# Kernel tuning notes

Measured on AMD Instinct MI355X. Metric: run time of the kernel, lower is better.

The kernel has to match this reference:

```python
import jax, jax.numpy as jnp
import numpy as np

MIN_EXPERT_CAPACITY = 4
EPS = 1e-9
CAPACITY_FACTOR = 2.0  # eval capacity factor


def cumsum_exclusive(t, axis):
    return jnp.cumsum(t, axis=axis) - t


def safe_one_hot(idx, depth):
    # one_hot with an extra slot so idx == depth maps to nothing, then slice
    return jax.nn.one_hot(idx, depth + 1)[..., :depth]


def setup_inputs() -> dict:
    key = jax.random.key(0)
    k_x, k_g, k_w1, k_w2 = jax.random.split(key, 4)
    b, n, d, e, h = 2, 4096, 512, 16, 2048
    x = jax.random.normal(k_x, (b, n, d), dtype=jnp.float32)
    w_gating = jax.random.normal(k_g, (d, e), dtype=jnp.float32) / np.sqrt(d)
    w1 = jax.random.normal(k_w1, (e, d, h), dtype=jnp.float32) / np.sqrt(d)
    w2 = jax.random.normal(k_w2, (e, h, d), dtype=jnp.float32) / np.sqrt(h)
    return {"x": x, "w_gating": w_gating, "w1": w1, "w2": w2}


def top2_gating(x, w_gating):
    b, n, d = x.shape
    e = w_gating.shape[-1]
    raw_gates = jax.nn.softmax(jnp.einsum('bnd,de->bne', x, w_gating), axis=-1)

    gate_1 = jnp.max(raw_gates, axis=-1)
    index_1 = jnp.argmax(raw_gates, axis=-1)
    mask_1 = jax.nn.one_hot(index_1, e, dtype=raw_gates.dtype)

    gates_without_top1 = raw_gates * (1.0 - mask_1)
    gate_2 = jnp.max(gates_without_top1, axis=-1)
    index_2 = jnp.argmax(gates_without_top1, axis=-1)
    mask_2 = jax.nn.one_hot(index_2, e, dtype=raw_gates.dtype)

    denom = gate_1 + gate_2 + EPS
    gate_1 = gate_1 / denom
    gate_2 = gate_2 / denom

    # load-balancing loss
    density_1 = jnp.mean(mask_1, axis=-2)
    density_1_proxy = jnp.mean(raw_gates, axis=-2)
    loss = jnp.mean(density_1_proxy * density_1) * float(e * e)

    # second policy == 'all' -> keep mask_2 as-is

    capacity = max(min(n, int((n * 2) * CAPACITY_FACTOR / e)), MIN_EXPERT_CAPACITY)
    cap_f = float(capacity)

    pos1 = cumsum_exclusive(mask_1, axis=-2) * mask_1  # [b,n,e]
    mask_1 = mask_1 * (pos1 < cap_f).astype(mask_1.dtype)
    mask_1_count = jnp.sum(mask_1, axis=-2, keepdims=True)
    mask_1_flat = jnp.sum(mask_1, axis=-1)  # [b,n]
    pos1 = jnp.sum(pos1, axis=-1)
    gate_1 = gate_1 * mask_1_flat

    pos2 = (cumsum_exclusive(mask_2, axis=-2) + mask_1_count) * mask_2
    mask_2 = mask_2 * (pos2 < cap_f).astype(mask_2.dtype)
    mask_2_flat = jnp.sum(mask_2, axis=-1)
    pos2 = jnp.sum(pos2, axis=-1)
    gate_2 = gate_2 * mask_2_flat

    # combine tensor: [b, n, e, c]
    combine = (gate_1[..., None, None] * mask_1_flat[..., None, None]
               * jax.nn.one_hot(index_1, e, dtype=x.dtype)[..., None]
               * safe_one_hot(pos1.astype(jnp.int32), capacity)[..., None, :]
               + gate_2[..., None, None] * mask_2_flat[..., None, None]
               * jax.nn.one_hot(index_2, e, dtype=x.dtype)[..., None]
               * safe_one_hot(pos2.astype(jnp.int32), capacity)[..., None, :])
    dispatch = (combine > 0).astype(combine.dtype)
    return dispatch, combine, loss


def reference(x, w_gating, w1, w2):
    dispatch, combine, loss = top2_gating(x, w_gating)
    # dispatch: gather tokens into expert buckets [e, b, c, d]
    expert_inputs = jnp.einsum('bnd,bnec->ebcd', x, dispatch)
    # expert FFN (eval mode: dropout is identity)
    hidden = jax.nn.relu(jnp.einsum('ebcd,edh->ebch', expert_inputs, w1))
    expert_outputs = jnp.einsum('ebch,ehd->ebcd', hidden, w2)
    # combine back to token order, weighted by gate values
    output = jnp.einsum('ebcd,bnec->bnd', expert_outputs, combine)
    return output
```

## Files before the change

### kernel.cpp

```cpp
#include <hip/hip_runtime.h>

#define BB 2
#define NN 4096
#define DD 512
#define EE 16
#define HH 2048
#define CAP 1024
#define NTOK (BB*NN)
#define MM (BB*CAP)
#define MAXSTRIP 160

typedef unsigned short ushort_t;
typedef __attribute__((ext_vector_type(8))) short bf16x8;
typedef __attribute__((ext_vector_type(4))) float floatx4;

__device__ __forceinline__ ushort_t f2bf(float f) {
    union { float f; unsigned u; } v; v.f = f;
    unsigned r = v.u + 0x7fffu + ((v.u >> 16) & 1u);
    return (ushort_t)(r >> 16);
}

__device__ __forceinline__ void cp16(const void* g, void* l) {
    __builtin_amdgcn_global_load_lds(
        (const __attribute__((address_space(1))) void*)g,
        (__attribute__((address_space(3))) void*)l, 16, 0, 0);
}

__launch_bounds__(256)
__global__ void gating_kernel(const float* __restrict__ x,
                              const float* __restrict__ wg,
                              int* __restrict__ e1, int* __restrict__ e2,
                              float* __restrict__ g1, float* __restrict__ g2,
                              ushort_t* __restrict__ xbf) {
    int wave = threadIdx.x >> 6;
    int lane = threadIdx.x & 63;
    int t = blockIdx.x * 4 + wave;
    const float* xp = x + (size_t)t * DD;

    float4 xa = ((const float4*)xp)[lane * 2];
    float4 xb = ((const float4*)xp)[lane * 2 + 1];
    float xs[8] = {xa.x, xa.y, xa.z, xa.w, xb.x, xb.y, xb.z, xb.w};

    ushort4 h0, h1;
    h0.x = f2bf(xs[0]); h0.y = f2bf(xs[1]); h0.z = f2bf(xs[2]); h0.w = f2bf(xs[3]);
    h1.x = f2bf(xs[4]); h1.y = f2bf(xs[5]); h1.z = f2bf(xs[6]); h1.w = f2bf(xs[7]);
    ushort4* xo = (ushort4*)(xbf + (size_t)t * DD);
    xo[lane * 2] = h0; xo[lane * 2 + 1] = h1;

    float acc[EE];
#pragma unroll
    for (int e = 0; e < EE; e++) acc[e] = 0.f;
    int d0 = lane * 8;
#pragma unroll
    for (int j = 0; j < 8; j++) {
        const float* wrow = wg + (d0 + j) * EE;
#pragma unroll
        for (int e = 0; e < EE; e++) acc[e] = fmaf(xs[j], wrow[e], acc[e]);
    }
#pragma unroll
    for (int off = 32; off > 0; off >>= 1) {
#pragma unroll
        for (int e = 0; e < EE; e++) acc[e] += __shfl_xor(acc[e], off, 64);
    }
    if (lane == 0) {
        float m = acc[0];
#pragma unroll
        for (int e = 1; e < EE; e++) m = fmaxf(m, acc[e]);
        float p[EE]; float s = 0.f;
#pragma unroll
        for (int e = 0; e < EE; e++) { p[e] = __expf(acc[e] - m); s += p[e]; }
        float inv = 1.f / s;
#pragma unroll
        for (int e = 0; e < EE; e++) p[e] *= inv;
        int i1 = 0; float v1 = p[0];
#pragma unroll
        for (int e = 1; e < EE; e++) if (p[e] > v1) { v1 = p[e]; i1 = e; }
        int i2 = (i1 == 0) ? 1 : 0; float v2 = p[i2];
#pragma unroll
        for (int e = 0; e < EE; e++)
            if (e != i1 && p[e] > v2) { v2 = p[e]; i2 = e; }
        float denom = v1 + v2 + 1e-9f;
        e1[t] = i1; e2[t] = i2;
        g1[t] = v1 / denom; g2[t] = v2 / denom;
    }
}

__launch_bounds__(256)
__global__ void scan_kernel(const int* __restrict__ e1, const int* __restrict__ e2,
                            const float* __restrict__ g1, const float* __restrict__ g2,
                            int* __restrict__ s2t, float* __restrict__ s2g,
                            int* __restrict__ used) {
    int b = blockIdx.x / EE;
    int e = blockIdx.x % EE;
    int tid = threadIdx.x;
    const int base = b * NN;
    int n0 = tid * 16;

    unsigned m1 = 0, m2 = 0;
    int c1 = 0, c2 = 0;
#pragma unroll
    for (int j = 0; j < 16; j++) {
        int n = n0 + j;
        if (e1[base + n] == e) { m1 |= 1u << j; c1++; }
        if (e2[base + n] == e) { m2 |= 1u << j; c2++; }
    }
    __shared__ int s1[256], s2[256];
    __shared__ int s_used;
    s1[tid] = c1; s2[tid] = c2;
    __syncthreads();
    for (int off = 1; off < 256; off <<= 1) {
        int a1 = (tid >= off) ? s1[tid - off] : 0;
        int a2 = (tid >= off) ? s2[tid - off] : 0;
        __syncthreads();
        s1[tid] += a1; s2[tid] += a2;
        __syncthreads();
    }
    int total1 = s1[255];
    int total2 = s2[255];
    int kept1 = min(total1, CAP);
    int ex1 = s1[tid] - c1;
    int ex2 = s2[tid] - c2 + kept1;
    const int sbase = (e * BB + b) * CAP;
#pragma unroll
    for (int j = 0; j < 16; j++) {
        int n = n0 + j;
        if (m1 & (1u << j)) {
            if (ex1 < CAP) { s2t[sbase + ex1] = base + n; s2g[sbase + ex1] = g1[base + n]; }
            ex1++;
        }
        if (m2 & (1u << j)) {
            if (ex2 < CAP) { s2t[sbase + ex2] = base + n; s2g[sbase + ex2] = g2[base + n]; }
            ex2++;
        }
    }
    if (tid == 255) {
        int kept2 = min(total2, max(0, CAP - kept1));
        int u = kept1 + kept2;
        used[e * BB + b] = u;
        s_used = u;
    }
    __syncthreads();
    for (int i = s_used + tid; i < CAP; i += 256) s2t[sbase + i] = -1;
}

__global__ void schedule_kernel(const int* __restrict__ used, int* __restrict__ meta) {
    __shared__ int ns[32], pre[32];
    int i = threadIdx.x;
    if (i < 32) {
        int e = i >> 1, b = i & 1;
        ns[i] = (used[e * BB + b] + 127) >> 7;
    }
    __syncthreads();
    if (i == 0) {
        int acc = 0;
        for (int j = 0; j < 32; j++) { pre[j] = acc; acc += ns[j]; }
    }
    __syncthreads();
    if (i < 16) {
        int e = i;
        int xcd = e & 7;
        int mine  = ns[2 * e] + ns[2 * e + 1];
        int po    = (e < 8) ? (e + 8) : (e - 8);
        int other = ns[2 * po] + ns[2 * po + 1];
        if (e < 8) {
            meta[xcd]     = (mine + other) * 16;
            meta[8 + xcd] = (mine + other) * 4;
        }
        int off = (e < 8) ? 0 : other;
        int* sc1 = meta + 16 + xcd * 512 + off * 16;
        int j = 0;
        for (int col = 0; col < 16; col++)
            for (int bb = 0; bb < 2; bb++)
                for (int s = 0; s < ns[2 * e + bb]; s++) {
                    int wi = pre[2 * e + bb] + s;
                    sc1[j++] = (e << 17) | (wi << 9) | ((bb * 8 + s) << 5) | col;
                }
        int* sc2 = meta + 16 + 4096 + xcd * 128 + off * 4;
        j = 0;
        for (int col = 0; col < 4; col++)
            for (int bb = 0; bb < 2; bb++)
                for (int s = 0; s < ns[2 * e + bb]; s++) {
                    int wi = pre[2 * e + bb] + s;
                    sc2[j++] = (e << 17) | (wi << 9) | ((bb * 8 + s) << 5) | col;
                }
    }
}

__global__ void transpose_bf16(const float* __restrict__ in,
                               ushort_t* __restrict__ outp, int R, int C) {
    __shared__ float tile[32][33];
    const float* slab = in + (size_t)blockIdx.z * R * C;
    ushort_t* oslab = outp + (size_t)blockIdx.z * R * C;
    int c0 = blockIdx.x * 32, r0 = blockIdx.y * 32;
    int tx = threadIdx.x, ty = threadIdx.y;
#pragma unroll
    for (int j = 0; j < 4; j++)
        tile[ty + j * 8][tx] = slab[(size_t)(r0 + ty + j * 8) * C + c0 + tx];
    __syncthreads();
#pragma unroll
    for (int j = 0; j < 4; j++)
        oslab[(size_t)(c0 + ty + j * 8) * R + r0 + tx] = f2bf(tile[tx][ty + j * 8]);
}

template <int MODE>
__launch_bounds__(256)
__global__ void gemm_mfma(const ushort_t* __restrict__ Abase,
                          const ushort_t* __restrict__ Bt,
                          void* __restrict__ Cout,
                          const int* __restrict__ meta,
                          const int* __restrict__ s2t,
                          const float* __restrict__ s2g) {
    constexpr int K = (MODE == 0) ? DD : HH;
    constexpr int KITERS = K / 32;

    int xcd = blockIdx.x;
    if ((int)blockIdx.y >= meta[(MODE == 0 ? 0 : 8) + xcd]) return;
    int job = meta[16 + (MODE == 0 ? 0 : 4096) + xcd * (MODE == 0 ? 512 : 128) + blockIdx.y];
    int col0  = (job & 31) * 128;
    int ytile = (job >> 5) & 15;
    int wi    = (job >> 9) & 255;
    int e     = job >> 17;

    __shared__ ushort_t As[2][128 * 32];
    __shared__ ushort_t Bs[2][128 * 32];

    int tid = threadIdx.x;
    int lane = tid & 63;
    int wid = tid >> 6;
    int wave_m = (wid & 1) << 6;
    int wave_n = (wid >> 1) << 6;
    int lm = lane & 15;
    int quad = lane >> 4;
    int sw = (quad ^ ((lm >> 1) & 3)) * 8;

    const ushort_t* ga[2];
    const ushort_t* gb[2];
#pragma unroll
    for (int it = 0; it < 2; it++) {
        int idx = it * 256 + tid;
        int r = idx >> 2;
        int cg = (idx & 3) ^ ((r >> 1) & 3);
        if (MODE == 0) {
            int tok = s2t[e * MM + ytile * 128 + r];
            if (tok < 0) tok = 0;
            ga[it] = Abase + (size_t)tok * DD + cg * 8;
        } else {
            ga[it] = Abase + (size_t)(wi * 128 + r) * HH + cg * 8;
        }
        gb[it] = Bt + (size_t)e * HH * DD + (size_t)(col0 + r) * K + cg * 8;
    }

    auto stage = [&](int buf, int ki) {
#pragma unroll
        for (int it = 0; it < 2; it++)
            cp16(ga[it] + ki * 32, &As[buf][(it * 256 + tid) * 8]);
#pragma unroll
        for (int it = 0; it < 2; it++)
            cp16(gb[it] + ki * 32, &Bs[buf][(it * 256 + tid) * 8]);
    };

    floatx4 acc[4][4];
#pragma unroll
    for (int i = 0; i < 4; i++)
#pragma unroll
        for (int j = 0; j < 4; j++)
            acc[i][j] = (floatx4)(0.f);

    stage(0, 0);
#pragma unroll 2
    for (int ki = 0; ki < KITERS; ki++) {
        int cur = ki & 1;
        if (ki + 1 < KITERS) {
            stage(cur ^ 1, ki + 1);
            asm volatile("s_waitcnt vmcnt(4)\ns_barrier" ::: "memory");
        } else {
            asm volatile("s_waitcnt vmcnt(0)\ns_barrier" ::: "memory");
        }
        bf16x8 af[4], bfr[4];
#pragma unroll
        for (int mt = 0; mt < 4; mt++)
            af[mt] = *(const bf16x8*)&As[cur][(wave_m + mt * 16 + lm) * 32 + sw];
#pragma unroll
        for (int nt = 0; nt < 4; nt++)
            bfr[nt] = *(const bf16x8*)&Bs[cur][(wave_n + nt * 16 + lm) * 32 + sw];
#pragma unroll
        for (int mt = 0; mt < 4; mt++)
#pragma unroll
            for (int nt = 0; nt < 4; nt++)
                acc[mt][nt] = __builtin_amdgcn_mfma_f32_16x16x32_bf16(
                    af[mt], bfr[nt], acc[mt][nt], 0, 0, 0);
        asm volatile("s_waitcnt lgkmcnt(0)\ns_barrier" ::: "memory");
    }

    if (MODE == 0) {
        ushort_t* hp = (ushort_t*)Cout + (size_t)wi * 128 * HH;
#pragma unroll
        for (int mt = 0; mt < 4; mt++) {
#pragma unroll
            for (int r = 0; r < 4; r++) {
                int row = wave_m + mt * 16 + quad * 4 + r;
#pragma unroll
                for (int nt = 0; nt < 4; nt++) {
                    int col = col0 + wave_n + nt * 16 + lm;
                    hp[(size_t)row * HH + col] = f2bf(fmaxf(acc[mt][nt][r], 0.f));
                }
            }
        }
    } else {
        float* outp = (float*)Cout;
#pragma unroll
        for (int mt = 0; mt < 4; mt++) {
#pragma unroll
            for (int r = 0; r < 4; r++) {
                int row = wave_m + mt * 16 + quad * 4 + r;
                int slot = e * MM + ytile * 128 + row;
                int tok = s2t[slot];
                if (tok < 0) continue;
                float g = s2g[slot];
#pragma unroll
                for (int nt = 0; nt < 4; nt++) {
                    int col = col0 + wave_n + nt * 16 + lm;
                    atomicAdd(outp + (size_t)tok * DD + col, g * acc[mt][nt][r]);
                }
            }
        }
    }
}

extern "C" void kernel_launch(void* const* d_in, const int* in_sizes, int n_in,
                              void* d_out, int out_size, void* d_ws, size_t ws_size,
                              hipStream_t stream) {
    const float* x  = (const float*)d_in[0];
    const float* wg = (const float*)d_in[1];
    const float* w1 = (const float*)d_in[2];
    const float* w2 = (const float*)d_in[3];
    float* out = (float*)d_out;

    char* ws = (char*)d_ws;
    int*      e1   = (int*)(ws);
    int*      e2   = (int*)(ws + 32768);
    float*    g1   = (float*)(ws + 65536);
    float*    g2   = (float*)(ws + 98304);
    int*      used = (int*)(ws + 131072);
    int*      meta = (int*)(ws + 132096);
    int*      s2t  = (int*)(ws + 152704);
    float*    s2g  = (float*)(ws + 283776);
    ushort_t* xbf  = (ushort_t*)(ws + 414848);
    ushort_t* wt   = (ushort_t*)(ws + 8803456);
    ushort_t* hid  = (ushort_t*)(ws + 42357888);

    hipMemsetAsync(out, 0, (size_t)NTOK * DD * sizeof(float), stream);

    gating_kernel<<<NTOK / 4, 256, 0, stream>>>(x, wg, e1, e2, g1, g2, xbf);
    scan_kernel<<<BB * EE, 256, 0, stream>>>(e1, e2, g1, g2, s2t, s2g, used);
    schedule_kernel<<<1, 64, 0, stream>>>(used, meta);

    transpose_bf16<<<dim3(HH / 32, DD / 32, EE), dim3(32, 8), 0, stream>>>(w1, wt, DD, HH);
    gemm_mfma<0><<<dim3(8, 512), 256, 0, stream>>>(xbf, wt, hid, meta, s2t, s2g);

    transpose_bf16<<<dim3(DD / 32, HH / 32, EE), dim3(32, 8), 0, stream>>>(w2, wt, HH, DD);
    gemm_mfma<1><<<dim3(8, 128), 256, 0, stream>>>(hid, wt, out, meta, s2t, s2g);
}
```

Before: 366.6 us.

## Fuse expert FFN GEMMs into one kernel keeping hidden chunks in LDS

Replaces the two separate expert GEMM launches, and the bf16 hidden tensor round trip through global memory, with one fused kernel. Each 512-thread block owns a 128-row token tile of one expert, computes 256-wide hidden chunks into swizzled LDS, and accumulates the second GEMM in registers. The schedule becomes one job per token tile, and the weight transpose uses 64x64 tiles with float2 loads. In exchange, the grid is far smaller (at most a few dozen active blocks), LDS use is large and the accumulators take many registers, so the GPU may be underused.

```diff
diff --git a/kernel.cpp b/kernel.cpp
--- a/kernel.cpp
+++ b/kernel.cpp
@@ -8,7 +8,6 @@
 #define CAP 1024
 #define NTOK (BB*NN)
 #define MM (BB*CAP)
-#define MAXSTRIP 160
 
 typedef unsigned short ushort_t;
 typedef __attribute__((ext_vector_type(8))) short bf16x8;
@@ -144,187 +143,203 @@
 }
 
 __global__ void schedule_kernel(const int* __restrict__ used, int* __restrict__ meta) {
-    __shared__ int ns[32], pre[32];
-    int i = threadIdx.x;
-    if (i < 32) {
-        int e = i >> 1, b = i & 1;
-        ns[i] = (used[e * BB + b] + 127) >> 7;
-    }
-    __syncthreads();
-    if (i == 0) {
-        int acc = 0;
-        for (int j = 0; j < 32; j++) { pre[j] = acc; acc += ns[j]; }
-    }
-    __syncthreads();
-    if (i < 16) {
-        int e = i;
-        int xcd = e & 7;
-        int mine  = ns[2 * e] + ns[2 * e + 1];
-        int po    = (e < 8) ? (e + 8) : (e - 8);
-        int other = ns[2 * po] + ns[2 * po + 1];
-        if (e < 8) {
-            meta[xcd]     = (mine + other) * 16;
-            meta[8 + xcd] = (mine + other) * 4;
-        }
-        int off = (e < 8) ? 0 : other;
-        int* sc1 = meta + 16 + xcd * 512 + off * 16;
-        int j = 0;
-        for (int col = 0; col < 16; col++)
-            for (int bb = 0; bb < 2; bb++)
-                for (int s = 0; s < ns[2 * e + bb]; s++) {
-                    int wi = pre[2 * e + bb] + s;
-                    sc1[j++] = (e << 17) | (wi << 9) | ((bb * 8 + s) << 5) | col;
-                }
-        int* sc2 = meta + 16 + 4096 + xcd * 128 + off * 4;
-        j = 0;
-        for (int col = 0; col < 4; col++)
-            for (int bb = 0; bb < 2; bb++)
-                for (int s = 0; s < ns[2 * e + bb]; s++) {
-                    int wi = pre[2 * e + bb] + s;
-                    sc2[j++] = (e << 17) | (wi << 9) | ((bb * 8 + s) << 5) | col;
-                }
-    }
+    int x = threadIdx.x;
+    if (x >= 8) return;
+    int cnt = 0;
+#pragma unroll
+    for (int ei = 0; ei < 2; ei++) {
+        int e = x + ei * 8;
+        for (int b = 0; b < 2; b++) {
+            int ns = (used[e * BB + b] + 127) >> 7;
+            for (int s = 0; s < ns; s++)
+                meta[8 + x * 32 + cnt++] = (e << 8) | ((e * BB + b) * 8 + s);
+        }
+    }
+    meta[x] = cnt;
 }
 
 __global__ void transpose_bf16(const float* __restrict__ in,
                                ushort_t* __restrict__ outp, int R, int C) {
-    __shared__ float tile[32][33];
+    __shared__ float tile[64][65];
     const float* slab = in + (size_t)blockIdx.z * R * C;
     ushort_t* oslab = outp + (size_t)blockIdx.z * R * C;
-    int c0 = blockIdx.x * 32, r0 = blockIdx.y * 32;
+    int c0 = blockIdx.x * 64, r0 = blockIdx.y * 64;
     int tx = threadIdx.x, ty = threadIdx.y;
 #pragma unroll
-    for (int j = 0; j < 4; j++)
-        tile[ty + j * 8][tx] = slab[(size_t)(r0 + ty + j * 8) * C + c0 + tx];
+    for (int j = 0; j < 8; j++) {
+        int r = ty + j * 8;
+        float2 v = *(const float2*)&slab[(size_t)(r0 + r) * C + c0 + tx * 2];
+        tile[r][tx * 2] = v.x; tile[r][tx * 2 + 1] = v.y;
+    }
     __syncthreads();
 #pragma unroll
-    for (int j = 0; j < 4; j++)
-        oslab[(size_t)(c0 + ty + j * 8) * R + r0 + tx] = f2bf(tile[tx][ty + j * 8]);
-}
-
-template <int MODE>
-__launch_bounds__(256)
-__global__ void gemm_mfma(const ushort_t* __restrict__ Abase,
-                          const ushort_t* __restrict__ Bt,
-                          void* __restrict__ Cout,
+    for (int j = 0; j < 8; j++) {
+        int c = ty + j * 8;
+        ushort2 h;
+        h.x = f2bf(tile[tx * 2][c]);
+        h.y = f2bf(tile[tx * 2 + 1][c]);
+        *(ushort2*)&oslab[(size_t)(c0 + c) * R + r0 + tx * 2] = h;
+    }
+}
+
+__launch_bounds__(512)
+__global__ void fused_ffn(const ushort_t* __restrict__ xbf,
+                          const ushort_t* __restrict__ w1t,
+                          const ushort_t* __restrict__ w2t,
+                          float* __restrict__ outp,
                           const int* __restrict__ meta,
                           const int* __restrict__ s2t,
                           const float* __restrict__ s2g) {
-    constexpr int K = (MODE == 0) ? DD : HH;
-    constexpr int KITERS = K / 32;
-
     int xcd = blockIdx.x;
-    if ((int)blockIdx.y >= meta[(MODE == 0 ? 0 : 8) + xcd]) return;
-    int job = meta[16 + (MODE == 0 ? 0 : 4096) + xcd * (MODE == 0 ? 512 : 128) + blockIdx.y];
-    int col0  = (job & 31) * 128;
-    int ytile = (job >> 5) & 15;
-    int wi    = (job >> 9) & 255;
-    int e     = job >> 17;
-
-    __shared__ ushort_t As[2][128 * 32];
-    __shared__ ushort_t Bs[2][128 * 32];
-
-    int tid = threadIdx.x;
-    int lane = tid & 63;
-    int wid = tid >> 6;
-    int wave_m = (wid & 1) << 6;
-    int wave_n = (wid >> 1) << 6;
-    int lm = lane & 15;
-    int quad = lane >> 4;
-    int sw = (quad ^ ((lm >> 1) & 3)) * 8;
-
-    const ushort_t* ga[2];
-    const ushort_t* gb[2];
-#pragma unroll
-    for (int it = 0; it < 2; it++) {
-        int idx = it * 256 + tid;
-        int r = idx >> 2;
-        int cg = (idx & 3) ^ ((r >> 1) & 3);
-        if (MODE == 0) {
-            int tok = s2t[e * MM + ytile * 128 + r];
-            if (tok < 0) tok = 0;
-            ga[it] = Abase + (size_t)tok * DD + cg * 8;
-        } else {
-            ga[it] = Abase + (size_t)(wi * 128 + r) * HH + cg * 8;
-        }
-        gb[it] = Bt + (size_t)e * HH * DD + (size_t)(col0 + r) * K + cg * 8;
-    }
-
-    auto stage = [&](int buf, int ki) {
-#pragma unroll
-        for (int it = 0; it < 2; it++)
-            cp16(ga[it] + ki * 32, &As[buf][(it * 256 + tid) * 8]);
-#pragma unroll
-        for (int it = 0; it < 2; it++)
-            cp16(gb[it] + ki * 32, &Bs[buf][(it * 256 + tid) * 8]);
-    };
-
-    floatx4 acc[4][4];
+    if ((int)blockIdx.y >= meta[xcd]) return;
+    int job = meta[8 + xcd * 32 + blockIdx.y];
+    int e = job >> 8;
+    int slot0 = (job & 255) << 7;
+
+    __shared__ ushort_t Ats[2][128 * 32];
+    __shared__ ushort_t Wts[2][512 * 32];
+    __shared__ ushort_t Hs[128 * 256];
+
+    const int tid = threadIdx.x;
+    const int lane = tid & 63;
+    const int wid = tid >> 6;
+    const int lm = lane & 15;
+    const int quad = lane >> 4;
+    const int swz = (quad ^ ((lm >> 1) & 3)) * 8;
+
+    const int mh   = (wid & 1) << 6;
+    const int g1_n = (wid >> 1) << 6;
+    const int g2_n = (wid >> 1) << 7;
+
+    int arow = tid >> 2;
+    int tokA = s2t[slot0 + arow];
+    const ushort_t* gA = xbf + (size_t)(tokA < 0 ? 0 : tokA) * DD
+                             + ((tid & 3) ^ ((arow >> 1) & 3)) * 8;
+    const ushort_t* w1b = w1t + ((size_t)e << 20);
+    const ushort_t* w2b = w2t + ((size_t)e << 20);
+    int r0 = tid >> 2, r1 = 128 + (tid >> 2);
+    const ushort_t* gW1a = w1b + (size_t)r0 * DD + ((tid & 3) ^ ((r0 >> 1) & 3)) * 8;
+    const ushort_t* gW1b = w1b + (size_t)r1 * DD + ((tid & 3) ^ ((r1 >> 1) & 3)) * 8;
+    const ushort_t* gW2[4];
+#pragma unroll
+    for (int it = 0; it < 4; it++) {
+        int r = it * 128 + (tid >> 2);
+        gW2[it] = w2b + (size_t)r * HH + ((tid & 3) ^ ((r >> 1) & 3)) * 8;
+    }
+
+    floatx4 acc[4][8];
 #pragma unroll
     for (int i = 0; i < 4; i++)
 #pragma unroll
-        for (int j = 0; j < 4; j++)
+        for (int j = 0; j < 8; j++)
             acc[i][j] = (floatx4)(0.f);
 
-    stage(0, 0);
-#pragma unroll 2
-    for (int ki = 0; ki < KITERS; ki++) {
-        int cur = ki & 1;
-        if (ki + 1 < KITERS) {
-            stage(cur ^ 1, ki + 1);
-            asm volatile("s_waitcnt vmcnt(4)\ns_barrier" ::: "memory");
-        } else {
-            asm volatile("s_waitcnt vmcnt(0)\ns_barrier" ::: "memory");
-        }
-        bf16x8 af[4], bfr[4];
+    for (int chunk = 0; chunk < HH / 256; chunk++) {
+        floatx4 acch[4][4];
+#pragma unroll
+        for (int i = 0; i < 4; i++)
+#pragma unroll
+            for (int j = 0; j < 4; j++)
+                acch[i][j] = (floatx4)(0.f);
+        {
+            const ushort_t* p1 = gW1a + ((size_t)chunk << 17);
+            const ushort_t* p2 = gW1b + ((size_t)chunk << 17);
+            cp16(gA, &Ats[0][tid * 8]);
+            cp16(p1, &Wts[0][tid * 8]);
+            cp16(p2, &Wts[0][(512 + tid) * 8]);
+            for (int kk = 0; kk < 16; kk++) {
+                int cur = kk & 1;
+                if (kk < 15) {
+                    int nx = cur ^ 1, ko = (kk + 1) * 32;
+                    cp16(gA + ko, &Ats[nx][tid * 8]);
+                    cp16(p1 + ko, &Wts[nx][tid * 8]);
+                    cp16(p2 + ko, &Wts[nx][(512 + tid) * 8]);
+                    asm volatile("s_waitcnt vmcnt(3)\ns_barrier" ::: "memory");
+                } else {
+                    asm volatile("s_waitcnt vmcnt(0)\ns_barrier" ::: "memory");
+                }
+                bf16x8 af[4];
+#pragma unroll
+                for (int mt = 0; mt < 4; mt++)
+                    af[mt] = *(const bf16x8*)&Ats[cur][(mh + mt * 16 + lm) * 32 + swz];
+#pragma unroll
+                for (int nt = 0; nt < 4; nt++) {
+                    bf16x8 bf = *(const bf16x8*)&Wts[cur][(g1_n + nt * 16 + lm) * 32 + swz];
+#pragma unroll
+                    for (int mt = 0; mt < 4; mt++)
+                        acch[mt][nt] = __builtin_amdgcn_mfma_f32_16x16x32_bf16(
+                            af[mt], bf, acch[mt][nt], 0, 0, 0);
+                }
+                asm volatile("s_waitcnt lgkmcnt(0)\ns_barrier" ::: "memory");
+            }
+        }
 #pragma unroll
         for (int mt = 0; mt < 4; mt++)
-            af[mt] = *(const bf16x8*)&As[cur][(wave_m + mt * 16 + lm) * 32 + sw];
-#pragma unroll
-        for (int nt = 0; nt < 4; nt++)
-            bfr[nt] = *(const bf16x8*)&Bs[cur][(wave_n + nt * 16 + lm) * 32 + sw];
-#pragma unroll
-        for (int mt = 0; mt < 4; mt++)
 #pragma unroll
             for (int nt = 0; nt < 4; nt++)
-                acc[mt][nt] = __builtin_amdgcn_mfma_f32_16x16x32_bf16(
-                    af[mt], bfr[nt], acc[mt][nt], 0, 0, 0);
+#pragma unroll
+                for (int r = 0; r < 4; r++) {
+                    int row = mh + mt * 16 + quad * 4 + r;
+                    int col = g1_n + nt * 16 + lm;
+                    int ch = (col >> 3) ^ (row & 15);
+                    Hs[row * 256 + ch * 8 + (col & 7)] =
+                        f2bf(fmaxf(acch[mt][nt][r], 0.f));
+                }
         asm volatile("s_waitcnt lgkmcnt(0)\ns_barrier" ::: "memory");
-    }
-
-    if (MODE == 0) {
-        ushort_t* hp = (ushort_t*)Cout + (size_t)wi * 128 * HH;
-#pragma unroll
-        for (int mt = 0; mt < 4; mt++) {
-#pragma unroll
-            for (int r = 0; r < 4; r++) {
-                int row = wave_m + mt * 16 + quad * 4 + r;
-#pragma unroll
-                for (int nt = 0; nt < 4; nt++) {
-                    int col = col0 + wave_n + nt * 16 + lm;
-                    hp[(size_t)row * HH + col] = f2bf(fmaxf(acc[mt][nt][r], 0.f));
-                }
+
+        {
+            size_t co = (size_t)chunk << 8;
+            cp16(gW2[0] + co, &Wts[0][tid * 8]);
+            cp16(gW2[1] + co, &Wts[0][(512 + tid) * 8]);
+            cp16(gW2[2] + co, &Wts[0][(1024 + tid) * 8]);
+            cp16(gW2[3] + co, &Wts[0][(1536 + tid) * 8]);
+            for (int kk = 0; kk < 8; kk++) {
+                int cur = kk & 1;
+                if (kk < 7) {
+                    int nx = cur ^ 1; size_t ko = co + (kk + 1) * 32;
+                    cp16(gW2[0] + ko, &Wts[nx][tid * 8]);
+                    cp16(gW2[1] + ko, &Wts[nx][(512 + tid) * 8]);
+                    cp16(gW2[2] + ko, &Wts[nx][(1024 + tid) * 8]);
+                    cp16(gW2[3] + ko, &Wts[nx][(1536 + tid) * 8]);
+                    asm volatile("s_waitcnt vmcnt(4)\ns_barrier" ::: "memory");
+                } else {
+                    asm volatile("s_waitcnt vmcnt(0)\ns_barrier" ::: "memory");
+                }
+                bf16x8 ah[4];
+#pragma unroll
+                for (int mt = 0; mt < 4; mt++) {
+                    int row = mh + mt * 16 + lm;
+                    int ch = ((kk << 2) + quad) ^ lm;
+                    ah[mt] = *(const bf16x8*)&Hs[row * 256 + ch * 8];
+                }
+#pragma unroll
+                for (int nt = 0; nt < 8; nt++) {
+                    bf16x8 bf = *(const bf16x8*)&Wts[cur][(g2_n + nt * 16 + lm) * 32 + swz];
+#pragma unroll
+                    for (int mt = 0; mt < 4; mt++)
+                        acc[mt][nt] = __builtin_amdgcn_mfma_f32_16x16x32_bf16(
+                            ah[mt], bf, acc[mt][nt], 0, 0, 0);
+                }
+                asm volatile("s_waitcnt lgkmcnt(0)\ns_barrier" ::: "memory");
             }
         }
-    } else {
-        float* outp = (float*)Cout;
-#pragma unroll
-        for (int mt = 0; mt < 4; mt++) {
-#pragma unroll
-            for (int r = 0; r < 4; r++) {
-                int row = wave_m + mt * 16 + quad * 4 + r;
-                int slot = e * MM + ytile * 128 + row;
-                int tok = s2t[slot];
-                if (tok < 0) continue;
-                float g = s2g[slot];
-#pragma unroll
-                for (int nt = 0; nt < 4; nt++) {
-                    int col = col0 + wave_n + nt * 16 + lm;
-                    atomicAdd(outp + (size_t)tok * DD + col, g * acc[mt][nt][r]);
-                }
+    }
+
+#pragma unroll
+    for (int mt = 0; mt < 4; mt++)
+#pragma unroll
+        for (int r = 0; r < 4; r++) {
+            int row = mh + mt * 16 + quad * 4 + r;
+            int slot = slot0 + row;
+            int tok = s2t[slot];
+            if (tok < 0) continue;
+            float g = s2g[slot];
+#pragma unroll
+            for (int nt = 0; nt < 8; nt++) {
+                int col = g2_n + nt * 16 + lm;
+                atomicAdd(outp + (size_t)tok * DD + col, g * acc[mt][nt][r]);
             }
         }
-    }
 }
 
 extern "C" void kernel_launch(void* const* d_in, const int* in_sizes, int n_in,
@@ -343,11 +358,11 @@
     float*    g2   = (float*)(ws + 98304);
     int*      used = (int*)(ws + 131072);
     int*      meta = (int*)(ws + 132096);
-    int*      s2t  = (int*)(ws + 152704);
-    float*    s2g  = (float*)(ws + 283776);
-    ushort_t* xbf  = (ushort_t*)(ws + 414848);
-    ushort_t* wt   = (ushort_t*)(ws + 8803456);
-    ushort_t* hid  = (ushort_t*)(ws + 42357888);
+    int*      s2t  = (int*)(ws + 136192);
+    float*    s2g  = (float*)(ws + 267264);
+    ushort_t* xbf  = (ushort_t*)(ws + 398336);
+    ushort_t* w1t  = (ushort_t*)(ws + 8786944);
+    ushort_t* w2t  = (ushort_t*)(ws + 42341376);
 
     hipMemsetAsync(out, 0, (size_t)NTOK * DD * sizeof(float), stream);
 
@@ -355,9 +370,8 @@
     scan_kernel<<<BB * EE, 256, 0, stream>>>(e1, e2, g1, g2, s2t, s2g, used);
     schedule_kernel<<<1, 64, 0, stream>>>(used, meta);
 
-    transpose_bf16<<<dim3(HH / 32, DD / 32, EE), dim3(32, 8), 0, stream>>>(w1, wt, DD, HH);
-    gemm_mfma<0><<<dim3(8, 512), 256, 0, stream>>>(xbf, wt, hid, meta, s2t, s2g);
-
-    transpose_bf16<<<dim3(DD / 32, HH / 32, EE), dim3(32, 8), 0, stream>>>(w2, wt, HH, DD);
-    gemm_mfma<1><<<dim3(8, 128), 256, 0, stream>>>(hid, wt, out, meta, s2t, s2g);
-}
+    transpose_bf16<<<dim3(HH / 64, DD / 64, EE), dim3(32, 8), 0, stream>>>(w1, w1t, DD, HH);
+    transpose_bf16<<<dim3(DD / 64, HH / 64, EE), dim3(32, 8), 0, stream>>>(w2, w2t, HH, DD);
+
+    fused_ffn<<<dim3(8, 32), 512, 0, stream>>>(xbf, w1t, w2t, out, meta, s2t, s2g);
+}
```

Result: slower. 508.5 us (+38.7%).
